# Kernel optimization log

Measured on AMD Instinct MI355X. Metric: run time of the kernel, lower is better.

Reference implementation:

```python
import jax, jax.numpy as jnp
import numpy as np

B, T, D_IN, UNITS = 64, 512, 1024, 1024


def setup_inputs() -> dict:
    key = jax.random.key(0)
    k1, k2, k3 = jax.random.split(key, 3)
    x = jax.random.normal(k1, (B, T, D_IN), dtype=jnp.float32)
    kernel = jax.random.normal(k2, (D_IN, UNITS), dtype=jnp.float32) * (1.0 / np.sqrt(D_IN))
    recurrent_kernel = jax.random.normal(k3, (UNITS, UNITS), dtype=jnp.float32) * (1.0 / np.sqrt(UNITS))
    return {"x": x, "kernel": kernel, "recurrent_kernel": recurrent_kernel}


def reference(x, kernel, recurrent_kernel):
    # Hoist input-to-hidden projection out of the time loop: [B,T,U]
    xk = jnp.einsum('btd,du->btu', x, kernel)

    def step(h, xk_t):
        # Elman step: h' = relu(x_t @ W + h @ U)
        h_new = jax.nn.relu(xk_t + h @ recurrent_kernel)
        return h_new, h_new

    h0 = jnp.zeros((x.shape[0], kernel.shape[1]), dtype=x.dtype)
    _, outs = jax.lax.scan(step, h0, jnp.swapaxes(xk, 0, 1))  # outs: [T,B,U]
    return jnp.swapaxes(outs, 0, 1)  # [B,T,U]
```

## Files before the change

### kernel.cpp

```cpp
#include <hip/hip_runtime.h>
#include <cstdint>
#include <cstddef>


typedef __attribute__((ext_vector_type(8))) short short8;
typedef __attribute__((ext_vector_type(4))) float f32x4;

static __device__ __forceinline__ unsigned short f2bf_rne(float f) {
  unsigned u = __float_as_uint(f);
  u += 0x7fffu + ((u >> 16) & 1u);
  return (unsigned short)(u >> 16);
}

static __device__ __forceinline__ void st_g16_cc(unsigned short* p, unsigned short val) {
  unsigned v32 = val;
  asm volatile("global_store_short %0, %1, off sc0 sc1"
               :: "v"(p), "v"(v32) : "memory");
}
static __device__ __forceinline__ void wait_vm0() {
  asm volatile("s_waitcnt vmcnt(0)" ::: "memory");
}
static __device__ __forceinline__ unsigned ld_flag_cc(const unsigned int* p) {
  unsigned v;
  asm volatile("global_load_dword %0, %1, off sc0 sc1\n\t"
               "s_waitcnt vmcnt(0)"
               : "=v"(v) : "v"(p) : "memory");
  return v;
}
static __device__ __forceinline__ void flag_add_cc(unsigned int* p, unsigned val) {
  asm volatile("global_atomic_add %0, %1, off sc1"
               :: "v"(p), "v"(val) : "memory");
}

__global__ __launch_bounds__(256) void xproj_kernel(const float* __restrict__ x,
                                                    const float* __restrict__ kern,
                                                    float* __restrict__ out) {
  __shared__ unsigned short Abuf[128 * 40];
  __shared__ unsigned short Bbuf[128 * 40];
  const int tid = threadIdx.x;
  const int lane = tid & 63;
  const int wv = tid >> 6;
  const int q = lane >> 4;
  const int lr = lane & 15;
  const int wm = (wv >> 1) * 64;
  const int wn = (wv & 1) * 64;
  const long rowbase = (long)blockIdx.y * 128;
  const int colbase = blockIdx.x * 128;

  f32x4 acc[4][4];
#pragma unroll
  for (int i = 0; i < 4; i++)
#pragma unroll
    for (int j = 0; j < 4; j++) acc[i][j] = (f32x4)0.f;

  for (int kb = 0; kb < 1024; kb += 32) {
#pragma unroll
    for (int r = 0; r < 4; ++r) {
      int idx = tid + r * 256;
      int m = idx >> 3;
      int kk = (idx & 7) * 4;
      float4 v = *(const float4*)(x + (rowbase + m) * 1024 + kb + kk);
      ushort4 w4;
      w4.x = f2bf_rne(v.x); w4.y = f2bf_rne(v.y);
      w4.z = f2bf_rne(v.z); w4.w = f2bf_rne(v.w);
      *(ushort4*)&Abuf[m * 40 + kk] = w4;
    }
#pragma unroll
    for (int r = 0; r < 4; ++r) {
      int idx = tid + r * 256;
      int kr = idx >> 5;
      int nn = (idx & 31) * 4;
      float4 v = *(const float4*)(kern + (long)(kb + kr) * 1024 + colbase + nn);
      Bbuf[(nn + 0) * 40 + kr] = f2bf_rne(v.x);
      Bbuf[(nn + 1) * 40 + kr] = f2bf_rne(v.y);
      Bbuf[(nn + 2) * 40 + kr] = f2bf_rne(v.z);
      Bbuf[(nn + 3) * 40 + kr] = f2bf_rne(v.w);
    }
    __syncthreads();
    short8 af[4], bfr[4];
#pragma unroll
    for (int i = 0; i < 4; i++)
      af[i] = *(const short8*)&Abuf[(wm + i * 16 + lr) * 40 + q * 8];
#pragma unroll
    for (int j = 0; j < 4; j++)
      bfr[j] = *(const short8*)&Bbuf[(wn + j * 16 + lr) * 40 + q * 8];
#pragma unroll
    for (int i = 0; i < 4; i++)
#pragma unroll
      for (int j = 0; j < 4; j++)
        acc[i][j] = __builtin_amdgcn_mfma_f32_16x16x32_bf16(af[i], bfr[j], acc[i][j], 0, 0, 0);
    __syncthreads();
  }
#pragma unroll
  for (int i = 0; i < 4; i++) {
#pragma unroll
    for (int r = 0; r < 4; r++) {
      long row = rowbase + wm + i * 16 + q * 4 + r;
      float* op = out + row * 1024 + colbase + wn + lr;
#pragma unroll
      for (int j = 0; j < 4; j++) op[j * 16] = acc[i][j][r];
    }
  }
}

__global__ __launch_bounds__(256) void rnn_scan_kernel(const float* __restrict__ R,
                                                       float* __restrict__ out,
                                                       unsigned short* __restrict__ hbuf,
                                                       unsigned int* __restrict__ flags) {
  const int tid = threadIdx.x;
  const int lane = tid & 63;
  const int wv = tid >> 6;
  const int q = lane >> 4;
  const int lr = lane & 15;
  const int cluster = blockIdx.x & 3;
  const int cg = blockIdx.x >> 2;

  short8 w[2][8];
#pragma unroll
  for (int nt = 0; nt < 2; nt++) {
    int col = cg * 32 + nt * 16 + lr;
#pragma unroll
    for (int cc = 0; cc < 8; cc++) {
      int k0 = wv * 256 + cc * 32 + q * 8;
      short8 t8;
#pragma unroll
      for (int j = 0; j < 8; j++)
        t8[j] = (short)f2bf_rne(R[(long)(k0 + j) * 1024 + col]);
      w[nt][cc] = t8;
    }
  }

  __shared__ float red[4 * 2 * 64 * 4];
  unsigned int* myflag = flags + cluster * 64;
  const int m_lo = tid >> 5;
  const int myn = tid & 31;
  const int off0 = (wv * 32 + q) * 128 + lr * 8;

  for (int t = 0; t < 512; ++t) {
    f32x4 acc0 = (f32x4)0.f, acc1 = (f32x4)0.f;
    if (t > 0) {
      const unsigned short* hb = hbuf + (size_t)((((t - 1) & 1) * 2 + 0) * 4 + cluster) * 16384;
      const unsigned short* lb = hbuf + (size_t)((((t - 1) & 1) * 2 + 1) * 4 + cluster) * 16384;
      const unsigned short* a0 = hb + off0;
      const unsigned short* a4 = a0 + 2048;
      const unsigned short* b0 = lb + off0;
      const unsigned short* b4 = b0 + 2048;
      short8 ah[8], al[8];
      asm volatile(
          "global_load_dwordx4 %0,  %16, off sc0 sc1\n\t"
          "global_load_dwordx4 %1,  %16, off offset:1024 sc0 sc1\n\t"
          "global_load_dwordx4 %2,  %16, off offset:2048 sc0 sc1\n\t"
          "global_load_dwordx4 %3,  %16, off offset:3072 sc0 sc1\n\t"
          "global_load_dwordx4 %4,  %17, off sc0 sc1\n\t"
          "global_load_dwordx4 %5,  %17, off offset:1024 sc0 sc1\n\t"
          "global_load_dwordx4 %6,  %17, off offset:2048 sc0 sc1\n\t"
          "global_load_dwordx4 %7,  %17, off offset:3072 sc0 sc1\n\t"
          "global_load_dwordx4 %8,  %18, off sc0 sc1\n\t"
          "global_load_dwordx4 %9,  %18, off offset:1024 sc0 sc1\n\t"
          "global_load_dwordx4 %10, %18, off offset:2048 sc0 sc1\n\t"
          "global_load_dwordx4 %11, %18, off offset:3072 sc0 sc1\n\t"
          "global_load_dwordx4 %12, %19, off sc0 sc1\n\t"
          "global_load_dwordx4 %13, %19, off offset:1024 sc0 sc1\n\t"
          "global_load_dwordx4 %14, %19, off offset:2048 sc0 sc1\n\t"
          "global_load_dwordx4 %15, %19, off offset:3072 sc0 sc1\n\t"
          "s_waitcnt vmcnt(0)"
          : "=&v"(ah[0]), "=&v"(ah[1]), "=&v"(ah[2]), "=&v"(ah[3]),
            "=&v"(ah[4]), "=&v"(ah[5]), "=&v"(ah[6]), "=&v"(ah[7]),
            "=&v"(al[0]), "=&v"(al[1]), "=&v"(al[2]), "=&v"(al[3]),
            "=&v"(al[4]), "=&v"(al[5]), "=&v"(al[6]), "=&v"(al[7])
          : "v"(a0), "v"(a4), "v"(b0), "v"(b4)
          : "memory");
#pragma unroll
      for (int cc = 0; cc < 8; cc++) {
        acc0 = __builtin_amdgcn_mfma_f32_16x16x32_bf16(ah[cc], w[0][cc], acc0, 0, 0, 0);
        acc0 = __builtin_amdgcn_mfma_f32_16x16x32_bf16(al[cc], w[0][cc], acc0, 0, 0, 0);
        acc1 = __builtin_amdgcn_mfma_f32_16x16x32_bf16(ah[cc], w[1][cc], acc1, 0, 0, 0);
        acc1 = __builtin_amdgcn_mfma_f32_16x16x32_bf16(al[cc], w[1][cc], acc1, 0, 0, 0);
      }
    }
    *(f32x4*)&red[((wv * 2 + 0) * 64 + lane) * 4] = acc0;
    *(f32x4*)&red[((wv * 2 + 1) * 64 + lane) * 4] = acc1;
    __syncthreads();
#pragma unroll
    for (int mi = 0; mi < 2; ++mi) {
      int m = m_lo + mi * 8;
      int nt = myn >> 4;
      int ln = (myn & 15) + ((m >> 2) & 3) * 16;
      int r = m & 3;
      float s = red[((0 * 2 + nt) * 64 + ln) * 4 + r] + red[((1 * 2 + nt) * 64 + ln) * 4 + r] +
                red[((2 * 2 + nt) * 64 + ln) * 4 + r] + red[((3 * 2 + nt) * 64 + ln) * 4 + r];
      long orow = (long)(cluster * 16 + m) * 512 + t;
      float* op = out + orow * 1024 + cg * 32 + myn;
      float h = s + *op;
      h = fmaxf(h, 0.0f);
      *op = h;
      unsigned short hi = f2bf_rne(h);
      float hf = __uint_as_float(((unsigned)hi) << 16);
      unsigned short lo = f2bf_rne(h - hf);
      int k = cg * 32 + myn;
      int off = (k >> 3) * 128 + m * 8 + (k & 7);
      st_g16_cc(hbuf + (size_t)(((t & 1) * 2 + 0) * 4 + cluster) * 16384 + off, hi);
      st_g16_cc(hbuf + (size_t)(((t & 1) * 2 + 1) * 4 + cluster) * 16384 + off, lo);
    }
    if (t < 511) {
      wait_vm0();
      __syncthreads();
      if (tid == 0) {
        flag_add_cc(myflag, 1u);
        unsigned target = 32u * (unsigned)(t + 1);
        while (ld_flag_cc(myflag) < target) {
          __builtin_amdgcn_s_sleep(1);
        }
      }
      __syncthreads();
    }
  }
}

extern "C" void kernel_launch(void* const* d_in, const int* in_sizes, int n_in,
                              void* d_out, int out_size, void* d_ws, size_t ws_size,
                              hipStream_t stream) {
  const float* x = (const float*)d_in[0];
  const float* kern = (const float*)d_in[1];
  const float* R = (const float*)d_in[2];
  float* out = (float*)d_out;

  unsigned short* hbuf = (unsigned short*)d_ws;
  unsigned int* flags = (unsigned int*)((char*)d_ws + (size_t)2 * 2 * 4 * 16384 * sizeof(unsigned short));
  hipMemsetAsync(flags, 0, 1024, stream);

  dim3 g1(8, 256), b1(256);
  xproj_kernel<<<g1, b1, 0, stream>>>(x, kern, out);
  rnn_scan_kernel<<<128, 256, 0, stream>>>(R, out, hbuf, flags);
}
```

Before: 2.293 ms.

## Replace atomic-counter grid barrier with per-wave flags polled by every wave

The per-step grid synchronization no longer uses one atomic counter per cluster plus two block barriers. Each wave now stores its own monotonic step flag, and at the start of the next step all waves poll the 128 flags of their cluster in parallel, two loads per lane. The reduction buffer is double-buffered so the trailing __syncthreads can go, and the xk value is prefetched before the wait so its load latency is hidden. The MFMA chain is also split into four independent accumulators to shorten dependency stalls. In exchange there is more polling traffic, since every wave spins on global memory, and a larger flag region.

```diff
diff --git a/kernel.cpp b/kernel.cpp
--- a/kernel.cpp
+++ b/kernel.cpp
@@ -20,16 +20,17 @@
 static __device__ __forceinline__ void wait_vm0() {
   asm volatile("s_waitcnt vmcnt(0)" ::: "memory");
 }
-static __device__ __forceinline__ unsigned ld_flag_cc(const unsigned int* p) {
-  unsigned v;
-  asm volatile("global_load_dword %0, %1, off sc0 sc1\n\t"
+static __device__ __forceinline__ void st_flag_cc(unsigned int* p, unsigned val) {
+  asm volatile("global_store_dword %0, %1, off sc0 sc1"
+               :: "v"(p), "v"(val) : "memory");
+}
+static __device__ __forceinline__ void ld2_flag_cc(const unsigned int* p0,
+                                                   const unsigned int* p1,
+                                                   unsigned& f0, unsigned& f1) {
+  asm volatile("global_load_dword %0, %2, off sc0 sc1\n\t"
+               "global_load_dword %1, %3, off sc0 sc1\n\t"
                "s_waitcnt vmcnt(0)"
-               : "=v"(v) : "v"(p) : "memory");
-  return v;
-}
-static __device__ __forceinline__ void flag_add_cc(unsigned int* p, unsigned val) {
-  asm volatile("global_atomic_add %0, %1, off sc1"
-               :: "v"(p), "v"(val) : "memory");
+               : "=&v"(f0), "=&v"(f1) : "v"(p0), "v"(p1) : "memory");
 }
 
 __global__ __launch_bounds__(256) void xproj_kernel(const float* __restrict__ x,
@@ -130,15 +131,32 @@
     }
   }
 
-  __shared__ float red[4 * 2 * 64 * 4];
-  unsigned int* myflag = flags + cluster * 64;
+  __shared__ float red[2][4 * 2 * 64 * 4];
+  unsigned int* cflags = flags + cluster * 512;
+  unsigned int* myflag = cflags + (cg * 4 + wv) * 4;
+  const unsigned int* pf0 = cflags + lane * 4;
+  const unsigned int* pf1 = cflags + (lane + 64) * 4;
   const int m_lo = tid >> 5;
   const int myn = tid & 31;
   const int off0 = (wv * 32 + q) * 128 + lr * 8;
 
   for (int t = 0; t < 512; ++t) {
+    float xk[2];
+#pragma unroll
+    for (int mi = 0; mi < 2; ++mi) {
+      int m = m_lo + mi * 8;
+      long orow = (long)(cluster * 16 + m) * 512 + t;
+      xk[mi] = out[orow * 1024 + cg * 32 + myn];
+    }
+
     f32x4 acc0 = (f32x4)0.f, acc1 = (f32x4)0.f;
     if (t > 0) {
+      const unsigned tgt = (unsigned)t;
+      for (;;) {
+        unsigned f0, f1;
+        ld2_flag_cc(pf0, pf1, f0, f1);
+        if (__all((f0 >= tgt) & (f1 >= tgt))) break;
+      }
       const unsigned short* hb = hbuf + (size_t)((((t - 1) & 1) * 2 + 0) * 4 + cluster) * 16384;
       const unsigned short* lb = hbuf + (size_t)((((t - 1) & 1) * 2 + 1) * 4 + cluster) * 16384;
       const unsigned short* a0 = hb + off0;
@@ -170,16 +188,20 @@
             "=&v"(al[4]), "=&v"(al[5]), "=&v"(al[6]), "=&v"(al[7])
           : "v"(a0), "v"(a4), "v"(b0), "v"(b4)
           : "memory");
+      f32x4 a0h = (f32x4)0.f, a0l = (f32x4)0.f, a1h = (f32x4)0.f, a1l = (f32x4)0.f;
 #pragma unroll
       for (int cc = 0; cc < 8; cc++) {
-        acc0 = __builtin_amdgcn_mfma_f32_16x16x32_bf16(ah[cc], w[0][cc], acc0, 0, 0, 0);
-        acc0 = __builtin_amdgcn_mfma_f32_16x16x32_bf16(al[cc], w[0][cc], acc0, 0, 0, 0);
-        acc1 = __builtin_amdgcn_mfma_f32_16x16x32_bf16(ah[cc], w[1][cc], acc1, 0, 0, 0);
-        acc1 = __builtin_amdgcn_mfma_f32_16x16x32_bf16(al[cc], w[1][cc], acc1, 0, 0, 0);
+        a0h = __builtin_amdgcn_mfma_f32_16x16x32_bf16(ah[cc], w[0][cc], a0h, 0, 0, 0);
+        a0l = __builtin_amdgcn_mfma_f32_16x16x32_bf16(al[cc], w[0][cc], a0l, 0, 0, 0);
+        a1h = __builtin_amdgcn_mfma_f32_16x16x32_bf16(ah[cc], w[1][cc], a1h, 0, 0, 0);
+        a1l = __builtin_amdgcn_mfma_f32_16x16x32_bf16(al[cc], w[1][cc], a1l, 0, 0, 0);
       }
-    }
-    *(f32x4*)&red[((wv * 2 + 0) * 64 + lane) * 4] = acc0;
-    *(f32x4*)&red[((wv * 2 + 1) * 64 + lane) * 4] = acc1;
+      acc0 = a0h + a0l;
+      acc1 = a1h + a1l;
+    }
+    float* rp = red[t & 1];
+    *(f32x4*)&rp[((wv * 2 + 0) * 64 + lane) * 4] = acc0;
+    *(f32x4*)&rp[((wv * 2 + 1) * 64 + lane) * 4] = acc1;
     __syncthreads();
 #pragma unroll
     for (int mi = 0; mi < 2; ++mi) {
@@ -187,11 +209,11 @@
       int nt = myn >> 4;
       int ln = (myn & 15) + ((m >> 2) & 3) * 16;
       int r = m & 3;
-      float s = red[((0 * 2 + nt) * 64 + ln) * 4 + r] + red[((1 * 2 + nt) * 64 + ln) * 4 + r] +
-                red[((2 * 2 + nt) * 64 + ln) * 4 + r] + red[((3 * 2 + nt) * 64 + ln) * 4 + r];
+      float s = rp[((0 * 2 + nt) * 64 + ln) * 4 + r] + rp[((1 * 2 + nt) * 64 + ln) * 4 + r] +
+                rp[((2 * 2 + nt) * 64 + ln) * 4 + r] + rp[((3 * 2 + nt) * 64 + ln) * 4 + r];
       long orow = (long)(cluster * 16 + m) * 512 + t;
       float* op = out + orow * 1024 + cg * 32 + myn;
-      float h = s + *op;
+      float h = s + xk[mi];
       h = fmaxf(h, 0.0f);
       *op = h;
       unsigned short hi = f2bf_rne(h);
@@ -204,15 +226,7 @@
     }
     if (t < 511) {
       wait_vm0();
-      __syncthreads();
-      if (tid == 0) {
-        flag_add_cc(myflag, 1u);
-        unsigned target = 32u * (unsigned)(t + 1);
-        while (ld_flag_cc(myflag) < target) {
-          __builtin_amdgcn_s_sleep(1);
-        }
-      }
-      __syncthreads();
+      if (lane == 0) st_flag_cc(myflag, (unsigned)(t + 1));
     }
   }
 }
@@ -227,7 +241,7 @@
 
   unsigned short* hbuf = (unsigned short*)d_ws;
   unsigned int* flags = (unsigned int*)((char*)d_ws + (size_t)2 * 2 * 4 * 16384 * sizeof(unsigned short));
-  hipMemsetAsync(flags, 0, 1024, stream);
+  hipMemsetAsync(flags, 0, 8192, stream);
 
   dim3 g1(8, 256), b1(256);
   xproj_kernel<<<g1, b1, 0, stream>>>(x, kern, out);
```

After: 2.456 ms. 7.1% more time.
